# Optimization experiments

Measured on AMD Instinct MI355X. Metric: run time of the kernel, lower is better.

The kernel has to match this reference:

```python
import jax, jax.numpy as jnp
import numpy as np

EPS = 1e-3  # keras LayerNormalization default epsilon
D_INNER = 64


def setup_inputs() -> dict:
    key = jax.random.key(0)
    ks = jax.random.split(key, 5)
    B, N, M, C = 4, 1024, 32, 128
    x = jax.random.normal(ks[0], (B, N, M, C), dtype=jnp.float32)
    # Glorot-uniform init bounds
    lim_qk = float(np.sqrt(6.0 / (C + D_INNER)))
    lim_v = float(np.sqrt(6.0 / (C + C)))
    w_q = jax.random.uniform(ks[1], (C, D_INNER), jnp.float32, -lim_qk, lim_qk)
    w_k = jax.random.uniform(ks[2], (C, D_INNER), jnp.float32, -lim_qk, lim_qk)
    w_v = jax.random.uniform(ks[3], (C, C), jnp.float32, -lim_v, lim_v)
    lam = jnp.full((C,), 0.1, dtype=jnp.float32)  # lam_init_eps default eps=0.1
    gamma = jnp.ones((C,), dtype=jnp.float32)
    beta = jnp.zeros((C,), dtype=jnp.float32)
    return {"x": x, "gamma": gamma, "beta": beta, "w_q": w_q, "w_k": w_k,
            "w_v": w_v, "lam": lam}


def reference(x, gamma, beta, w_q, w_k, w_v, lam):
    # LayerNorm over channel axis C
    mean = jnp.mean(x, axis=-1, keepdims=True)
    var = jnp.mean(jnp.square(x - mean), axis=-1, keepdims=True)
    xn = (x - mean) * jax.lax.rsqrt(var + EPS) * gamma + beta  # [B,N,M,C]
    xn = jnp.transpose(xn, (0, 2, 1, 3))  # [B,M,N,C] attention over N per feature
    q = jnp.einsum('bmnc,cd->bmnd', xn, w_q)
    k = jnp.einsum('bmnc,cd->bmnd', xn, w_k)
    scores = jnp.einsum('bmnd,bmkd->bmnk', q, k) / jnp.sqrt(
        jnp.asarray(D_INNER, dtype=jnp.float32))
    A = jax.nn.softmax(scores, axis=-1)  # [B,M,N,N]
    v = jnp.einsum('bmnc,ce->bmne', xn, w_v)  # [B,M,N,C]
    attn = jnp.einsum('bmnk,bmkc->bmnc', A, v)
    attn = jnp.transpose(attn, (0, 2, 1, 3))  # back to [B,N,M,C]
    return x + attn * lam
```

## Files before the change

kernel.cpp:

```cpp
#include <hip/hip_runtime.h>
#include <hip/hip_bf16.h>

#define B_ 4
#define N_ 1024
#define M_ 32
#define C_ 128
#define D_ 64
#define BM_ (B_*M_)

typedef float f32x4 __attribute__((ext_vector_type(4)));
typedef float f32x16 __attribute__((ext_vector_type(16)));
typedef short short8 __attribute__((ext_vector_type(8)));
typedef short short4v __attribute__((ext_vector_type(4)));

#define EXP2(x) __builtin_amdgcn_exp2f(x)

static __device__ __forceinline__ int cvtpk_bf16(float lo, float hi) {
  int r;
  asm("v_cvt_pk_bf16_f32 %0, %1, %2" : "=v"(r) : "v"(lo), "v"(hi));
  return r;
}
static __device__ __forceinline__ void plswap(int& a, int& b) {
  asm("v_permlane32_swap_b32 %0, %1" : "+v"(a), "+v"(b));
}

__global__ __launch_bounds__(256) void prep_weights(
    const float* __restrict__ wq, const float* __restrict__ wk,
    const float* __restrict__ wv, __hip_bfloat16* __restrict__ wt) {
  int idx = blockIdx.x * 256 + threadIdx.x;
  int col = idx >> 7;
  int kk  = idx & 127;
  float v;
  if (col < 64)        v = wq[kk * 64 + col] * (0.125f * 1.44269504088896f);
  else if (col < 128)  v = wk[kk * 64 + (col - 64)];
  else                 v = wv[kk * 128 + (col - 128)];
  wt[col * 128 + kk] = __float2bfloat16(v);
}

__global__ __launch_bounds__(512, 6) void ln_qkv(
    const float* __restrict__ x, const float* __restrict__ gamma,
    const float* __restrict__ beta, const __hip_bfloat16* __restrict__ wt,
    __hip_bfloat16* __restrict__ q, __hip_bfloat16* __restrict__ k,
    __hip_bfloat16* __restrict__ vt) {
  __shared__ alignas(16) __hip_bfloat16 xn[128][136];

  int bid = blockIdx.x;
  int bm  = bid >> 3;
  int n0  = (bid & 7) * 128;
  int b   = bm >> 5, m = bm & 31;
  int tid = threadIdx.x;

  const float* xbase = x + ((((size_t)b * N_ + n0) * M_ + m) * C_);
  int c4 = tid & 31;
  float4 vch[8];
  #pragma unroll
  for (int it = 0; it < 8; ++it) {
    int r = (it * 512 + tid) >> 5;
    vch[it] = *reinterpret_cast<const float4*>(xbase + (size_t)r * (M_ * C_) + c4 * 4);
  }
  float4 g4 = *reinterpret_cast<const float4*>(gamma + c4 * 4);
  float4 b4 = *reinterpret_cast<const float4*>(beta + c4 * 4);

  #pragma unroll
  for (int it = 0; it < 8; ++it) {
    int r = (it * 512 + tid) >> 5;
    float4 v = vch[it];
    float s  = (v.x + v.y) + (v.z + v.w);
    float sq = (v.x * v.x + v.y * v.y) + (v.z * v.z + v.w * v.w);
    s  += __shfl_xor(s, 1);  sq += __shfl_xor(sq, 1);
    s  += __shfl_xor(s, 2);  sq += __shfl_xor(sq, 2);
    s  += __shfl_xor(s, 4);  sq += __shfl_xor(sq, 4);
    s  += __shfl_xor(s, 8);  sq += __shfl_xor(sq, 8);
    s  += __shfl_xor(s, 16); sq += __shfl_xor(sq, 16);
    float mean = s * (1.f / 128.f);
    float var  = sq * (1.f / 128.f) - mean * mean;
    float rstd = rsqrtf(var + 1e-3f);
    alignas(8) __hip_bfloat16 tmp[4];
    tmp[0] = __float2bfloat16((v.x - mean) * rstd * g4.x + b4.x);
    tmp[1] = __float2bfloat16((v.y - mean) * rstd * g4.y + b4.y);
    tmp[2] = __float2bfloat16((v.z - mean) * rstd * g4.z + b4.z);
    tmp[3] = __float2bfloat16((v.w - mean) * rstd * g4.w + b4.w);
    *reinterpret_cast<short4v*>(&xn[r][c4 * 4]) =
        *reinterpret_cast<const short4v*>(tmp);
  }
  __syncthreads();

  int w = tid >> 6, l = tid & 63, lr = l & 15, lh = l >> 4;
  int ct0 = w, ct1 = w + 8;

  short8 wf0[4], wf1[4];
  #pragma unroll
  for (int h = 0; h < 4; ++h) {
    wf0[h] = *reinterpret_cast<const short8*>(
        &wt[(ct0 * 16 + lr) * 128 + h * 32 + lh * 8]);
    wf1[h] = *reinterpret_cast<const short8*>(
        &wt[(ct1 * 16 + lr) * 128 + h * 32 + lh * 8]);
  }

  const f32x4 fzero = {0.f, 0.f, 0.f, 0.f};
  int col0 = ct0 * 16 + lr;
  int cV   = w * 16 + lr;
  #pragma unroll
  for (int rt = 0; rt < 8; ++rt) {
    short8 a[4];
    #pragma unroll
    for (int h = 0; h < 4; ++h)
      a[h] = *reinterpret_cast<const short8*>(&xn[rt * 16 + lr][h * 32 + lh * 8]);
    f32x4 acc0 = fzero, acc1 = fzero;
    #pragma unroll
    for (int h = 0; h < 4; ++h) {
      acc0 = __builtin_amdgcn_mfma_f32_16x16x32_bf16(a[h], wf0[h], acc0, 0, 0, 0);
      acc1 = __builtin_amdgcn_mfma_f32_16x16x32_bf16(a[h], wf1[h], acc1, 0, 0, 0);
    }
    int nb = n0 + rt * 16 + lh * 4;
    if (ct0 < 4) {
      #pragma unroll
      for (int r = 0; r < 4; ++r)
        q[((size_t)bm * N_ + nb + r) * D_ + col0] = __float2bfloat16(acc0[r]);
    } else {
      #pragma unroll
      for (int r = 0; r < 4; ++r)
        k[((size_t)bm * N_ + nb + r) * D_ + (col0 - 64)] = __float2bfloat16(acc0[r]);
    }
    alignas(8) __hip_bfloat16 tmp[4];
    #pragma unroll
    for (int r = 0; r < 4; ++r) tmp[r] = __float2bfloat16(acc1[r]);
    *reinterpret_cast<short4v*>(&vt[((size_t)bm * C_ + cV) * N_ + nb]) =
        *reinterpret_cast<const short4v*>(tmp);
  }
}

__global__ __launch_bounds__(256, 2) void attn_kernel(
    const float* __restrict__ x, const float* __restrict__ lam,
    const __hip_bfloat16* __restrict__ q, const __hip_bfloat16* __restrict__ k,
    const __hip_bfloat16* __restrict__ vt, float* __restrict__ out) {
  __shared__ alignas(16) __hip_bfloat16 kbuf[2][64 * 72];
  __shared__ alignas(16) __hip_bfloat16 vbuf[2][128 * 72];

  int h   = blockIdx.x;
  int s_  = h >> 3;
  int bm  = (s_ >> 3) * 8 + (h & 7);
  int n0  = (s_ & 7) * 128;
  int b   = bm >> 5, m = bm & 31;
  int tid = threadIdx.x;
  int w = tid >> 6, l = tid & 63;
  int lq = l & 31, hi = l >> 5;

  const __hip_bfloat16* kbase = k + (size_t)bm * N_ * D_;
  const __hip_bfloat16* vbase = vt + (size_t)bm * C_ * N_;

  int kr0 = tid >> 3,          kc0 = tid & 7;
  int kr1 = (tid + 256) >> 3,  kc1 = tid & 7;
  int vr[4], vc = tid & 7;
  #pragma unroll
  for (int i = 0; i < 4; ++i) vr[i] = (tid + i * 256) >> 3;

  short8 qf[4];
  {
    int n = n0 + w * 32 + lq;
    const __hip_bfloat16* qp = q + ((size_t)bm * N_ + n) * D_;
    #pragma unroll
    for (int s = 0; s < 4; ++s)
      qf[s] = *reinterpret_cast<const short8*>(qp + s * 16 + hi * 8);
  }

  f32x16 acc[4];
  const f32x16 z16 = {0.f,0.f,0.f,0.f,0.f,0.f,0.f,0.f,
                      0.f,0.f,0.f,0.f,0.f,0.f,0.f,0.f};
  #pragma unroll
  for (int ct = 0; ct < 4; ++ct) acc[ct] = z16;
  float m_run = -1e30f, l_run = 0.f;

  short8 kreg[2], vreg[4];
  kreg[0] = *reinterpret_cast<const short8*>(&kbase[(size_t)kr0 * D_ + kc0 * 8]);
  kreg[1] = *reinterpret_cast<const short8*>(&kbase[(size_t)kr1 * D_ + kc1 * 8]);
  #pragma unroll
  for (int i = 0; i < 4; ++i)
    vreg[i] = *reinterpret_cast<const short8*>(&vbase[(size_t)vr[i] * N_ + vc * 8]);
  *reinterpret_cast<short8*>(&kbuf[0][kr0 * 72 + kc0 * 8]) = kreg[0];
  *reinterpret_cast<short8*>(&kbuf[0][kr1 * 72 + kc1 * 8]) = kreg[1];
  #pragma unroll
  for (int i = 0; i < 4; ++i)
    *reinterpret_cast<short8*>(&vbuf[0][vr[i] * 72 + vc * 8]) = vreg[i];
  __syncthreads();

  for (int t = 0; t < 16; ++t) {
    int cur = t & 1;
    if (t < 15) {
      int j0n = (t + 1) * 64;
      kreg[0] = *reinterpret_cast<const short8*>(&kbase[(size_t)(j0n + kr0) * D_ + kc0 * 8]);
      kreg[1] = *reinterpret_cast<const short8*>(&kbase[(size_t)(j0n + kr1) * D_ + kc1 * 8]);
      #pragma unroll
      for (int i = 0; i < 4; ++i)
        vreg[i] = *reinterpret_cast<const short8*>(&vbase[(size_t)vr[i] * N_ + j0n + vc * 8]);
    }

    const __hip_bfloat16* kt  = kbuf[cur];
    const __hip_bfloat16* vtt = vbuf[cur];

    f32x16 st[2];
    st[0] = z16; st[1] = z16;
    #pragma unroll
    for (int s = 0; s < 4; ++s) {
      short8 kf0 = *reinterpret_cast<const short8*>(&kt[lq * 72 + s * 16 + hi * 8]);
      st[0] = __builtin_amdgcn_mfma_f32_32x32x16_bf16(kf0, qf[s], st[0], 0, 0, 0);
      short8 kf1 = *reinterpret_cast<const short8*>(&kt[(32 + lq) * 72 + s * 16 + hi * 8]);
      st[1] = __builtin_amdgcn_mfma_f32_32x32x16_bf16(kf1, qf[s], st[1], 0, 0, 0);
    }

    float mx;
    {
      float t8[8];
      #pragma unroll
      for (int i = 0; i < 8; ++i)
        t8[i] = fmaxf(fmaxf(st[0][i], st[0][i + 8]), fmaxf(st[1][i], st[1][i + 8]));
      float a0 = fmaxf(fmaxf(t8[0], t8[1]), fmaxf(t8[2], t8[3]));
      float a1 = fmaxf(fmaxf(t8[4], t8[5]), fmaxf(t8[6], t8[7]));
      mx = fmaxf(a0, a1);
      mx = fmaxf(mx, __shfl_xor(mx, 32));
    }
    if (__any(mx > m_run + 8.0f)) {
      float mnew = fmaxf(m_run, mx);
      float fac = EXP2(m_run - mnew);
      l_run *= fac;
      m_run = mnew;
      #pragma unroll
      for (int reg = 0; reg < 16; ++reg) {
        int qi = (reg & 3) + 8 * (reg >> 2) + 4 * hi;
        float f = __shfl(fac, qi);
        #pragma unroll
        for (int ct = 0; ct < 4; ++ct) acc[ct][reg] *= f;
      }
    }
    #pragma unroll
    for (int i = 0; i < 16; ++i) {
      st[0][i] = EXP2(st[0][i] - m_run);
      st[1][i] = EXP2(st[1][i] - m_run);
    }
    {
      float s8[8];
      #pragma unroll
      for (int i = 0; i < 8; ++i)
        s8[i] = (st[0][i] + st[0][i + 8]) + (st[1][i] + st[1][i + 8]);
      float rs = ((s8[0] + s8[1]) + (s8[2] + s8[3])) +
                 ((s8[4] + s8[5]) + (s8[6] + s8[7]));
      rs += __shfl_xor(rs, 32);
      l_run += rs;
    }

    union W4 { int w[4]; short8 s8; } pf[4];
    #pragma unroll
    for (int t32 = 0; t32 < 2; ++t32) {
      int A = cvtpk_bf16(st[t32][0], st[t32][1]);
      int Bw = cvtpk_bf16(st[t32][2], st[t32][3]);
      int Cw = cvtpk_bf16(st[t32][4], st[t32][5]);
      int Dw = cvtpk_bf16(st[t32][6], st[t32][7]);
      plswap(A, Cw);
      plswap(Bw, Dw);
      pf[t32 * 2].w[0] = A;  pf[t32 * 2].w[1] = Bw;
      pf[t32 * 2].w[2] = Cw; pf[t32 * 2].w[3] = Dw;
      int E = cvtpk_bf16(st[t32][8], st[t32][9]);
      int F = cvtpk_bf16(st[t32][10], st[t32][11]);
      int G = cvtpk_bf16(st[t32][12], st[t32][13]);
      int H = cvtpk_bf16(st[t32][14], st[t32][15]);
      plswap(E, G);
      plswap(F, H);
      pf[t32 * 2 + 1].w[0] = E; pf[t32 * 2 + 1].w[1] = F;
      pf[t32 * 2 + 1].w[2] = G; pf[t32 * 2 + 1].w[3] = H;
    }

    #pragma unroll
    for (int kb = 0; kb < 4; ++kb) {
      #pragma unroll
      for (int ct = 0; ct < 4; ++ct) {
        short8 vf = *reinterpret_cast<const short8*>(
            &vtt[(ct * 32 + lq) * 72 + kb * 16 + hi * 8]);
        acc[ct] = __builtin_amdgcn_mfma_f32_32x32x16_bf16(pf[kb].s8, vf, acc[ct], 0, 0, 0);
      }
    }

    if (t < 15) {
      int nxt = cur ^ 1;
      *reinterpret_cast<short8*>(&kbuf[nxt][kr0 * 72 + kc0 * 8]) = kreg[0];
      *reinterpret_cast<short8*>(&kbuf[nxt][kr1 * 72 + kc1 * 8]) = kreg[1];
      #pragma unroll
      for (int i = 0; i < 4; ++i)
        *reinterpret_cast<short8*>(&vbuf[nxt][vr[i] * 72 + vc * 8]) = vreg[i];
      __syncthreads();
    }
  }

  float inv = 1.0f / l_run;
  float rlv[16];
  #pragma unroll
  for (int reg = 0; reg < 16; ++reg) {
    int qi = (reg & 3) + 8 * (reg >> 2) + 4 * hi;
    rlv[reg] = __shfl(inv, qi);
  }
  #pragma unroll
  for (int ct = 0; ct < 4; ++ct) {
    int c = ct * 32 + lq;
    float lamc = lam[c];
    #pragma unroll
    for (int reg = 0; reg < 16; ++reg) {
      int qi = (reg & 3) + 8 * (reg >> 2) + 4 * hi;
      int n = n0 + w * 32 + qi;
      size_t idx = ((((size_t)b * N_ + n) * M_ + m) * C_) + c;
      out[idx] = x[idx] + acc[ct][reg] * rlv[reg] * lamc;
    }
  }
}

extern "C" void kernel_launch(void* const* d_in, const int* in_sizes, int n_in,
                              void* d_out, int out_size, void* d_ws, size_t ws_size,
                              hipStream_t stream) {
  const float* x     = (const float*)d_in[0];
  const float* gamma = (const float*)d_in[1];
  const float* beta  = (const float*)d_in[2];
  const float* wq    = (const float*)d_in[3];
  const float* wk    = (const float*)d_in[4];
  const float* wv    = (const float*)d_in[5];
  const float* lam   = (const float*)d_in[6];
  float* out = (float*)d_out;

  __hip_bfloat16* ws = (__hip_bfloat16*)d_ws;
  __hip_bfloat16* wt = ws;
  __hip_bfloat16* q  = wt + 256 * 128;
  __hip_bfloat16* k  = q + (size_t)BM_ * N_ * D_;
  __hip_bfloat16* vt = k + (size_t)BM_ * N_ * D_;

  prep_weights<<<128, 256, 0, stream>>>(wq, wk, wv, wt);
  ln_qkv<<<BM_ * (N_ / 128), 512, 0, stream>>>(x, gamma, beta, wt, q, k, vt);
  attn_kernel<<<BM_ * (N_ / 128), 256, 0, stream>>>(x, lam, q, k, vt, out);
}
```

Baseline: 111.7 us.

## Load V tiles directly into LDS with XOR-swizzled layout and MFMA priority

```diff
diff --git a/kernel.cpp b/kernel.cpp
--- a/kernel.cpp
+++ b/kernel.cpp
@@ -17,11 +17,22 @@
 
 static __device__ __forceinline__ int cvtpk_bf16(float lo, float hi) {
   int r;
-  asm("v_cvt_pk_bf16_f32 %0, %1, %2" : "=v"(r) : "v"(lo), "v"(hi));
+  asm volatile("v_cvt_pk_bf16_f32 %0, %1, %2" : "=v"(r) : "v"(lo), "v"(hi));
   return r;
 }
 static __device__ __forceinline__ void plswap(int& a, int& b) {
-  asm("v_permlane32_swap_b32 %0, %1" : "+v"(a), "+v"(b));
+  asm volatile("v_permlane32_swap_b32 %0, %1" : "+v"(a), "+v"(b));
+}
+
+static __device__ __forceinline__ int swz(int row, int chunk) {
+  return row * 64 + ((chunk ^ (row & 7)) << 3);
+}
+
+static __device__ __forceinline__ void gload_lds16(const __hip_bfloat16* g,
+                                                   __hip_bfloat16* l) {
+  __builtin_amdgcn_global_load_lds(
+      (const __attribute__((address_space(1))) void*)g,
+      (__attribute__((address_space(3))) void*)l, 16, 0, 0);
 }
 
 __global__ __launch_bounds__(256) void prep_weights(
@@ -135,7 +146,7 @@
     const __hip_bfloat16* __restrict__ q, const __hip_bfloat16* __restrict__ k,
     const __hip_bfloat16* __restrict__ vt, float* __restrict__ out) {
   __shared__ alignas(16) __hip_bfloat16 kbuf[2][64 * 72];
-  __shared__ alignas(16) __hip_bfloat16 vbuf[2][128 * 72];
+  __shared__ alignas(16) __hip_bfloat16 vbuf[2][128 * 64];
 
   int h   = blockIdx.x;
   int s_  = h >> 3;
@@ -149,11 +160,16 @@
   const __hip_bfloat16* kbase = k + (size_t)bm * N_ * D_;
   const __hip_bfloat16* vbase = vt + (size_t)bm * C_ * N_;
 
-  int kr0 = tid >> 3,          kc0 = tid & 7;
-  int kr1 = (tid + 256) >> 3,  kc1 = tid & 7;
-  int vr[4], vc = tid & 7;
-  #pragma unroll
-  for (int i = 0; i < 4; ++i) vr[i] = (tid + i * 256) >> 3;
+  int kr0 = tid >> 3,         kc = tid & 7;
+  int kr1 = (tid + 256) >> 3;
+
+  int vrow[4], vchk[4];
+  #pragma unroll
+  for (int p = 0; p < 4; ++p) {
+    int r = (w * 4 + p) * 8 + (l >> 3);
+    vrow[p] = r;
+    vchk[p] = (l & 7) ^ (r & 7);
+  }
 
   short8 qf[4];
   {
@@ -171,28 +187,27 @@
   for (int ct = 0; ct < 4; ++ct) acc[ct] = z16;
   float m_run = -1e30f, l_run = 0.f;
 
-  short8 kreg[2], vreg[4];
-  kreg[0] = *reinterpret_cast<const short8*>(&kbase[(size_t)kr0 * D_ + kc0 * 8]);
-  kreg[1] = *reinterpret_cast<const short8*>(&kbase[(size_t)kr1 * D_ + kc1 * 8]);
-  #pragma unroll
-  for (int i = 0; i < 4; ++i)
-    vreg[i] = *reinterpret_cast<const short8*>(&vbase[(size_t)vr[i] * N_ + vc * 8]);
-  *reinterpret_cast<short8*>(&kbuf[0][kr0 * 72 + kc0 * 8]) = kreg[0];
-  *reinterpret_cast<short8*>(&kbuf[0][kr1 * 72 + kc1 * 8]) = kreg[1];
-  #pragma unroll
-  for (int i = 0; i < 4; ++i)
-    *reinterpret_cast<short8*>(&vbuf[0][vr[i] * 72 + vc * 8]) = vreg[i];
+  short8 kreg[2];
+  kreg[0] = *reinterpret_cast<const short8*>(&kbase[(size_t)kr0 * D_ + kc * 8]);
+  kreg[1] = *reinterpret_cast<const short8*>(&kbase[(size_t)kr1 * D_ + kc * 8]);
+  #pragma unroll
+  for (int p = 0; p < 4; ++p)
+    gload_lds16(&vbase[(size_t)vrow[p] * N_ + vchk[p] * 8],
+                &vbuf[0][(w * 4 + p) * 512]);
+  *reinterpret_cast<short8*>(&kbuf[0][kr0 * 72 + kc * 8]) = kreg[0];
+  *reinterpret_cast<short8*>(&kbuf[0][kr1 * 72 + kc * 8]) = kreg[1];
   __syncthreads();
 
   for (int t = 0; t < 16; ++t) {
-    int cur = t & 1;
+    int cur = t & 1, nxt = cur ^ 1;
     if (t < 15) {
       int j0n = (t + 1) * 64;
-      kreg[0] = *reinterpret_cast<const short8*>(&kbase[(size_t)(j0n + kr0) * D_ + kc0 * 8]);
-      kreg[1] = *reinterpret_cast<const short8*>(&kbase[(size_t)(j0n + kr1) * D_ + kc1 * 8]);
-      #pragma unroll
-      for (int i = 0; i < 4; ++i)
-        vreg[i] = *reinterpret_cast<const short8*>(&vbase[(size_t)vr[i] * N_ + j0n + vc * 8]);
+      #pragma unroll
+      for (int p = 0; p < 4; ++p)
+        gload_lds16(&vbase[(size_t)vrow[p] * N_ + j0n + vchk[p] * 8],
+                    &vbuf[nxt][(w * 4 + p) * 512]);
+      kreg[0] = *reinterpret_cast<const short8*>(&kbase[(size_t)(j0n + kr0) * D_ + kc * 8]);
+      kreg[1] = *reinterpret_cast<const short8*>(&kbase[(size_t)(j0n + kr1) * D_ + kc * 8]);
     }
 
     const __hip_bfloat16* kt  = kbuf[cur];
@@ -269,23 +284,21 @@
       pf[t32 * 2 + 1].w[2] = G; pf[t32 * 2 + 1].w[3] = H;
     }
 
+    __builtin_amdgcn_s_setprio(1);
     #pragma unroll
     for (int kb = 0; kb < 4; ++kb) {
       #pragma unroll
       for (int ct = 0; ct < 4; ++ct) {
         short8 vf = *reinterpret_cast<const short8*>(
-            &vtt[(ct * 32 + lq) * 72 + kb * 16 + hi * 8]);
+            &vtt[swz(ct * 32 + lq, kb * 2 + hi)]);
         acc[ct] = __builtin_amdgcn_mfma_f32_32x32x16_bf16(pf[kb].s8, vf, acc[ct], 0, 0, 0);
       }
     }
+    __builtin_amdgcn_s_setprio(0);
 
     if (t < 15) {
-      int nxt = cur ^ 1;
-      *reinterpret_cast<short8*>(&kbuf[nxt][kr0 * 72 + kc0 * 8]) = kreg[0];
-      *reinterpret_cast<short8*>(&kbuf[nxt][kr1 * 72 + kc1 * 8]) = kreg[1];
-      #pragma unroll
-      for (int i = 0; i < 4; ++i)
-        *reinterpret_cast<short8*>(&vbuf[nxt][vr[i] * 72 + vc * 8]) = vreg[i];
+      *reinterpret_cast<short8*>(&kbuf[nxt][kr0 * 72 + kc * 8]) = kreg[0];
+      *reinterpret_cast<short8*>(&kbuf[nxt][kr1 * 72 + kc * 8]) = kreg[1];
       __syncthreads();
     }
   }
```

Result: slower. 114.1 us (+2.1%).
